# Kernel optimization log

Hardware: AMD Instinct MI355X
Metric: run time of the kernel (lower is better)

## Reference

```python
import jax, jax.numpy as jnp
import numpy as np

TOL = 1e-3

def _mask(x):
    # forward = relu, backward = identity (straight-through)
    return x + jax.lax.stop_gradient(jax.nn.relu(x) - x)

def setup_inputs() -> dict:
    key = jax.random.key(0)
    ks = jax.random.split(key, 6)
    B, L, A, Y = 4096, 64, 64, 128
    return {
        "LT": jax.random.uniform(ks[0], (B, L), jnp.float32),
        "K": jax.random.uniform(ks[1], (L, A), jnp.float32),
        "AT": jax.random.uniform(ks[2], (A,), jnp.float32),
        "u": jax.random.uniform(ks[3], (L * A, Y), jnp.float32),
        "e": jax.random.uniform(ks[4], (A, Y), jnp.float32),
        "b": jax.random.uniform(ks[5], (Y,), jnp.float32),
        "max_step": 50,
    }

def _fixed_point(LT3, AT3, Km, max_step):
    # LT3: [B,L,1], AT3: [A,1] (broadcasts over batch), Km: [L,A]
    B = LT3.shape[0]
    A = Km.shape[1]
    L = Km.shape[0]
    AF0 = jnp.zeros((B, A, 1), LT3.dtype)
    LF0 = jnp.zeros((B, L, 1), LT3.dtype)

    def step_fn(AF, LF):
        Ldi = LT3 / (jnp.matmul(Km, AF) + 1.0)          # [B,L,1]
        Adi = AT3 / (jnp.matmul(Km.T, LF) + 1.0)        # [B,A,1]
        AF_n = AT3 / (jnp.matmul(Km.T, Ldi) + 1.0)      # [B,A,1]
        LF_n = LT3 / (jnp.matmul(Km, Adi) + 1.0)        # [B,L,1]
        return AF_n, LF_n

    def cond(state):
        step, _, _, err = state
        return jnp.logical_and(step < max_step, err >= TOL)

    def body(state):
        step, AF, LF, _ = state
        AF_n, LF_n = step_fn(AF, LF)
        err = (jnp.max(jnp.abs(AF_n - AF) / (AF + 1e-5)) +
               jnp.max(jnp.abs(LF_n - LF) / (LF + 1e-5)))
        return (step + 1, AF_n, LF_n, err)

    _, AF, LF, _ = jax.lax.while_loop(cond, body, (0, AF0, LF0, jnp.array(jnp.inf, LT3.dtype)))
    return AF, LF

def reference(LT, K, AT, u, e, b, max_step):
    Km = _mask(K)            # [L,A]
    ATm = _mask(AT)          # [A]
    B = LT.shape[0]
    LT3 = LT[:, :, None]     # [B,L,1]
    AT3 = ATm[:, None]       # [A,1]

    # fixed-point loop was under torch.no_grad(): feed stop_gradient'd values
    AF, LF = _fixed_point(jax.lax.stop_gradient(LT3),
                          jax.lax.stop_gradient(AT3),
                          jax.lax.stop_gradient(Km), max_step)

    # final differentiable refinement step
    Ldi = LT3 / (jnp.matmul(Km, AF) + 1.0)
    Adi = AT3 / (jnp.matmul(Km.T, LF) + 1.0)
    AFf = AT3 / (jnp.matmul(Km.T, Ldi) + 1.0)   # [B,A,1]
    LFf = LT3 / (jnp.matmul(Km, Adi) + 1.0)     # [B,L,1]

    AFt = jnp.swapaxes(AFf, 1, 2)               # [B,1,A]
    D = (Km * jnp.matmul(LFf, AFt)).reshape(B, -1)   # [B, L*A]
    AFsq = AFt[:, 0, :]                          # [B,A]
    y = D @ u + AFsq @ e + b[None, :]            # [B,Y]
    return y
```

## Files before the change

### kernel.cpp

```cpp
#include <hip/hip_runtime.h>
#include <hip/hip_bf16.h>

typedef __bf16 bf16x8 __attribute__((ext_vector_type(8)));
typedef __bf16 bf16x4 __attribute__((ext_vector_type(4)));
typedef float  float4v __attribute__((ext_vector_type(4)));

#define MFMA16 __builtin_amdgcn_mfma_f32_16x16x32_bf16

__device__ __forceinline__ float bf2f(unsigned short u){
  union { unsigned int i; float f; } x; x.i = ((unsigned int)u) << 16; return x.f;
}
__device__ __forceinline__ unsigned short f2bf(float f){
  union { float f; unsigned int i; } x; x.f = f;
  unsigned int r = x.i + 0x7FFFu + ((x.i >> 16) & 1u);
  return (unsigned short)(r >> 16);
}
__device__ __forceinline__ float ldin(const void* p, int i, bool isbf){
  return isbf ? bf2f(((const unsigned short*)p)[i]) : ((const float*)p)[i];
}
__device__ __forceinline__ float frcp(float x){ return __builtin_amdgcn_rcpf(x); }

#define W2T_STRIDE 4160

__global__ __launch_bounds__(256) void k_prep(
    const void* K, const void* AT, const void* u, const void* e,
    const int* msin, __bf16* KmHi, __bf16* KTHi, __bf16* W2T, int* meta)
{
  int tid = threadIdx.x, bid = blockIdx.x;
  int ok = 0;
  if (tid < 64){
    float v = bf2f(((const unsigned short*)AT)[tid]);
    ok = (v >= 0.f && v <= 1.0f) ? 1 : 0;
  }
  int cnt = __syncthreads_count(ok);
  bool isbf = (cnt >= 60);

  if (bid < 256){
    int k0 = (bid >> 2) * 64, y0 = (bid & 3) * 32;
    __shared__ float sT[64 * 33];
    #pragma unroll
    for (int i = 0; i < 8; ++i){
      int flat = i * 256 + tid;
      int r = flat >> 5, c = flat & 31;
      sT[r * 33 + c] = ldin(u, (k0 + r) * 128 + (y0 + c), isbf);
    }
    __syncthreads();
    int l = k0 >> 6;
    #pragma unroll
    for (int i = 0; i < 8; ++i){
      int flat = i * 256 + tid;
      int yl = flat >> 6, kl = flat & 63;
      float km = ldin(K, l * 64 + kl, isbf); km = km > 0.f ? km : 0.f;
      W2T[(y0 + yl) * W2T_STRIDE + (k0 + kl)] = (__bf16)(km * sT[kl * 33 + yl]);
    }
  } else if (bid == 256){
    __shared__ float sK[64 * 65];
    #pragma unroll
    for (int i = 0; i < 16; ++i){
      int idx = i * 256 + tid;
      int l = idx >> 6, a = idx & 63;
      float v = ldin(K, idx, isbf); v = v > 0.f ? v : 0.f;
      sK[l * 65 + a] = v;
      KmHi[idx] = (__bf16)v;
    }
    __syncthreads();
    #pragma unroll
    for (int i = 0; i < 16; ++i){
      int idx = i * 256 + tid;
      int a = idx >> 6, l2 = idx & 63;
      KTHi[idx] = (__bf16)sK[l2 * 65 + a];
    }
    if (tid == 0){
      meta[0] = isbf ? 1 : 0;
      int mi = msin[0];
      if (mi <= 0 || mi > 1000000){
        float mf = ((const float*)msin)[0];
        mi = (mf > 0.f && mf < 1.0e6f) ? (int)mf : 50;
      }
      meta[1] = mi;
    }
  } else {
    __shared__ float sE[64 * 133];
    #pragma unroll
    for (int i = 0; i < 32; ++i){
      int idx = i * 256 + tid;
      int a = idx >> 7, y = idx & 127;
      sE[a * 133 + y] = ldin(e, idx, isbf);
    }
    __syncthreads();
    #pragma unroll
    for (int i = 0; i < 32; ++i){
      int idx = i * 256 + tid;
      int y = idx >> 6, a = idx & 63;
      W2T[y * W2T_STRIDE + 4096 + a] = (__bf16)sE[a * 133 + y];
    }
  }
}

template<bool SPLIT>
__device__ __forceinline__ void halfstep(
    const bf16x8 (&A)[4][2], const float4v (&V)[4],
    __bf16* sH, __bf16* sL, int rb, int wb)
{
  bf16x8 bh0 = *(const bf16x8*)(sH + rb);
  bf16x8 bh1 = *(const bf16x8*)(sH + rb + 32);
  const float4v ones = {1.f, 1.f, 1.f, 1.f};
  float4v c[4];
  #pragma unroll
  for (int T = 0; T < 4; ++T) c[T] = MFMA16(A[T][0], bh0, ones, 0, 0, 0);
  #pragma unroll
  for (int T = 0; T < 4; ++T) c[T] = MFMA16(A[T][1], bh1, c[T], 0, 0, 0);
  if (SPLIT){
    bf16x8 bl0 = *(const bf16x8*)(sL + rb);
    bf16x8 bl1 = *(const bf16x8*)(sL + rb + 32);
    const float4v zero = {0.f, 0.f, 0.f, 0.f};
    float4v d[4];
    #pragma unroll
    for (int T = 0; T < 4; ++T) d[T] = MFMA16(A[T][0], bl0, zero, 0, 0, 0);
    #pragma unroll
    for (int T = 0; T < 4; ++T) d[T] = MFMA16(A[T][1], bl1, d[T], 0, 0, 0);
    #pragma unroll
    for (int T = 0; T < 4; ++T) c[T] += d[T];
  }
  #pragma unroll
  for (int T = 0; T < 4; ++T){
    bf16x4 h, lo;
    #pragma unroll
    for (int r = 0; r < 4; ++r){
      float o = V[T][r] * frcp(c[T][r]);
      __bf16 hh = (__bf16)o;
      h[r] = hh;
      if (SPLIT) lo[r] = (__bf16)(o - (float)hh);
    }
    *(bf16x4*)(sH + wb + 16 * T) = h;
    if (SPLIT) *(bf16x4*)(sL + wb + 16 * T) = lo;
  }
}

__global__ __launch_bounds__(128, 1) void k_iter(
    const void* LT, const void* AT, const __bf16* KmHi, const __bf16* KTHi,
    const int* meta, __bf16* gAF, __bf16* gLF)
{
  __shared__ __attribute__((aligned(16))) __bf16 sHi[2][16 * 72];
  __shared__ __attribute__((aligned(16))) __bf16 sLo[2][16 * 72];
  const int tid = threadIdx.x, w = tid >> 6, lane = tid & 63;
  const int lr = lane & 15, q = lane >> 4;
  const int row0 = blockIdx.x * 16;
  __bf16* sH = sHi[w];
  __bf16* sL = sLo[w];

  const bf16x4 z4 = {(__bf16)0.f, (__bf16)0.f, (__bf16)0.f, (__bf16)0.f};
  for (int i = lane; i < 288; i += 64){
    *(bf16x4*)(sH + 4 * i) = z4;
    *(bf16x4*)(sL + 4 * i) = z4;
  }

  const int isbf = meta[0];
  const int ms   = meta[1];

  const __bf16* M1 = w ? KTHi : KmHi;
  const __bf16* M2 = w ? KmHi : KTHi;
  bf16x8 a1[4][2], a2[4][2];
  #pragma unroll
  for (int T = 0; T < 4; ++T)
    #pragma unroll
    for (int ks = 0; ks < 2; ++ks){
      int o = (16 * T + lr) * 64 + ks * 32 + q * 8;
      a1[T][ks] = *(const bf16x8*)(M1 + o);
      a2[T][ks] = *(const bf16x8*)(M2 + o);
    }

  float4v ltv[4], atv[4];
  if (isbf){
    const unsigned short* lt = (const unsigned short*)LT + (row0 + lr) * 64;
    const unsigned short* at = (const unsigned short*)AT;
    #pragma unroll
    for (int T = 0; T < 4; ++T)
      #pragma unroll
      for (int r = 0; r < 4; ++r){
        int d = 16 * T + q * 4 + r;
        ltv[T][r] = bf2f(lt[d]);
        atv[T][r] = fmaxf(bf2f(at[d]), 0.f);
      }
  } else {
    const float* lt = (const float*)LT + (row0 + lr) * 64;
    const float* at = (const float*)AT;
    #pragma unroll
    for (int T = 0; T < 4; ++T){
      ltv[T] = *(const float4v*)(lt + 16 * T + q * 4);
      float4v a = *(const float4v*)(at + 16 * T + q * 4);
      #pragma unroll
      for (int r = 0; r < 4; ++r) atv[T][r] = fmaxf(a[r], 0.f);
    }
  }
  float4v V1[4], V2[4];
  #pragma unroll
  for (int T = 0; T < 4; ++T){
    V1[T] = w ? atv[T] : ltv[T];
    V2[T] = w ? ltv[T] : atv[T];
  }

  const int rb = lr * 72 + q * 8;
  const int wb = lr * 72 + q * 4;

  const int nPlain = ms > 6 ? ms - 6 : 0;
  const int nSplit = ms - nPlain + 1;
  for (int s = 0; s < nPlain; ++s){
    halfstep<false>(a1, V1, sH, sL, rb, wb);
    halfstep<false>(a2, V2, sH, sL, rb, wb);
  }
  for (int s = 0; s < nSplit; ++s){
    halfstep<true>(a1, V1, sH, sL, rb, wb);
    halfstep<true>(a2, V2, sH, sL, rb, wb);
  }

  __bf16* gX = (w ? gLF : gAF) + row0 * 64;
  const int lrow = lane >> 2, seg = lane & 3;
  bf16x8 v0 = *(const bf16x8*)(sH + lrow * 72 + seg * 16);
  bf16x8 v1 = *(const bf16x8*)(sH + lrow * 72 + seg * 16 + 8);
  *(bf16x8*)(gX + lrow * 64 + seg * 16) = v0;
  *(bf16x8*)(gX + lrow * 64 + seg * 16 + 8) = v1;
}

__global__ __launch_bounds__(256) void k_epi(
    const __bf16* gAF, const __bf16* gLF, const __bf16* W2T,
    const void* bvec, const int* meta, void* out)
{
  __shared__ __attribute__((aligned(16))) __bf16 sAF[32 * 72], sLF[32 * 72];
  const int tid = threadIdx.x, wave = tid >> 6, lane = tid & 63;
  const int lr = lane & 15, q = lane >> 4;
  const int rg = blockIdx.x >> 1, yh = blockIdx.x & 1;
  const int row0 = rg * 32;
  const int isbf = meta[0];
  {
    int lrow = tid >> 3, seg = tid & 7;
    *(bf16x8*)(sAF + lrow * 72 + seg * 8) =
        *(const bf16x8*)(gAF + (row0 + lrow) * 64 + seg * 8);
    *(bf16x8*)(sLF + lrow * 72 + seg * 8) =
        *(const bf16x8*)(gLF + (row0 + lrow) * 64 + seg * 8);
  }
  __syncthreads();

  const int r0 = (wave & 1) * 16;
  const int y0 = yh * 64 + (wave >> 1) * 32;
  const int rloc = r0 + lr;

  const float bv0 = ldin(bvec, y0 + lr, isbf);
  const float bv1 = ldin(bvec, y0 + 16 + lr, isbf);
  float4v acc0 = {bv0, bv0, bv0, bv0};
  float4v acc1 = {bv1, bv1, bv1, bv1};

  bf16x8 af0 = *(const bf16x8*)(sAF + rloc * 72 + q * 8);
  bf16x8 af1 = *(const bf16x8*)(sAF + rloc * 72 + 32 + q * 8);
  float af0f[8], af1f[8];
  #pragma unroll
  for (int j = 0; j < 8; ++j){ af0f[j] = (float)af0[j]; af1f[j] = (float)af1[j]; }

  const __bf16* w0 = W2T + (y0 + lr) * W2T_STRIDE + q * 8;
  const __bf16* w1 = w0 + 16 * W2T_STRIDE;

  #pragma unroll 4
  for (int l = 0; l < 64; ++l){
    const float lf = (float)sLF[rloc * 72 + l];
    bf16x8 aD0, aD1;
    #pragma unroll
    for (int j = 0; j < 8; ++j){
      aD0[j] = (__bf16)(lf * af0f[j]);
      aD1[j] = (__bf16)(lf * af1f[j]);
    }
    const int kb = l * 64;
    bf16x8 b00 = *(const bf16x8*)(w0 + kb);
    bf16x8 b10 = *(const bf16x8*)(w1 + kb);
    bf16x8 b01 = *(const bf16x8*)(w0 + kb + 32);
    bf16x8 b11 = *(const bf16x8*)(w1 + kb + 32);
    acc0 = MFMA16(aD0, b00, acc0, 0, 0, 0);
    acc1 = MFMA16(aD0, b10, acc1, 0, 0, 0);
    acc0 = MFMA16(aD1, b01, acc0, 0, 0, 0);
    acc1 = MFMA16(aD1, b11, acc1, 0, 0, 0);
  }
  {
    bf16x8 b00 = *(const bf16x8*)(w0 + 4096);
    bf16x8 b10 = *(const bf16x8*)(w1 + 4096);
    bf16x8 b01 = *(const bf16x8*)(w0 + 4096 + 32);
    bf16x8 b11 = *(const bf16x8*)(w1 + 4096 + 32);
    acc0 = MFMA16(af0, b00, acc0, 0, 0, 0);
    acc1 = MFMA16(af0, b10, acc1, 0, 0, 0);
    acc0 = MFMA16(af1, b01, acc0, 0, 0, 0);
    acc1 = MFMA16(af1, b11, acc1, 0, 0, 0);
  }

  const int orow = row0 + r0 + q * 4;
  if (isbf){
    unsigned short* o = (unsigned short*)out;
    #pragma unroll
    for (int r = 0; r < 4; ++r){
      o[(orow + r) * 128 + y0 + lr]      = f2bf(acc0[r]);
      o[(orow + r) * 128 + y0 + 16 + lr] = f2bf(acc1[r]);
    }
  } else {
    float* o = (float*)out;
    #pragma unroll
    for (int r = 0; r < 4; ++r){
      o[(orow + r) * 128 + y0 + lr]      = acc0[r];
      o[(orow + r) * 128 + y0 + 16 + lr] = acc1[r];
    }
  }
}

extern "C" void kernel_launch(void* const* d_in, const int* in_sizes, int n_in,
                              void* d_out, int out_size, void* d_ws, size_t ws_size,
                              hipStream_t stream){
  char* ws = (char*)d_ws;
  int*    meta = (int*)ws;
  __bf16* KmHi = (__bf16*)(ws + 1024);
  __bf16* KTHi = (__bf16*)(ws + 9216);
  __bf16* gAF  = (__bf16*)(ws + 17408);
  __bf16* gLF  = (__bf16*)(ws + 541696);
  __bf16* W2T  = (__bf16*)(ws + 1065984);

  k_prep<<<dim3(258), dim3(256), 0, stream>>>(
      d_in[1], d_in[2], d_in[3], d_in[4], (const int*)d_in[6],
      KmHi, KTHi, W2T, meta);
  k_iter<<<dim3(256), dim3(128), 0, stream>>>(
      d_in[0], d_in[2], KmHi, KTHi, meta, gAF, gLF);
  k_epi<<<dim3(256), dim3(256), 0, stream>>>(
      gAF, gLF, W2T, d_in[5], meta, d_out);
}
```

Baseline: 142.4 us.

## Fuse prep into iteration kernel and double row tile in epilogue GEMM

The separate prep kernel is removed. Its work moves into extra blocks of the iteration kernel: W2T construction runs in blocks 256-385, and each iteration block builds its own Km/KmT fragments from shared memory, dropping one launch and the meta round-trip. The epilogue now processes 64 rows per block with two row tiles per wave, which reuses each W2T fragment load across twice as many MFMAs and halves the grid. Each epilogue block re-derives the dtype flag from the bias vector, and each iteration block redundantly reloads and transposes K.

```diff
diff --git a/kernel.cpp b/kernel.cpp
--- a/kernel.cpp
+++ b/kernel.cpp
@@ -6,6 +6,7 @@
 typedef float  float4v __attribute__((ext_vector_type(4)));
 
 #define MFMA16 __builtin_amdgcn_mfma_f32_16x16x32_bf16
+#define W2T_STRIDE 4160
 
 __device__ __forceinline__ float bf2f(unsigned short u){
   union { unsigned int i; float f; } x; x.i = ((unsigned int)u) << 16; return x.f;
@@ -20,82 +21,6 @@
 }
 __device__ __forceinline__ float frcp(float x){ return __builtin_amdgcn_rcpf(x); }
 
-#define W2T_STRIDE 4160
-
-__global__ __launch_bounds__(256) void k_prep(
-    const void* K, const void* AT, const void* u, const void* e,
-    const int* msin, __bf16* KmHi, __bf16* KTHi, __bf16* W2T, int* meta)
-{
-  int tid = threadIdx.x, bid = blockIdx.x;
-  int ok = 0;
-  if (tid < 64){
-    float v = bf2f(((const unsigned short*)AT)[tid]);
-    ok = (v >= 0.f && v <= 1.0f) ? 1 : 0;
-  }
-  int cnt = __syncthreads_count(ok);
-  bool isbf = (cnt >= 60);
-
-  if (bid < 256){
-    int k0 = (bid >> 2) * 64, y0 = (bid & 3) * 32;
-    __shared__ float sT[64 * 33];
-    #pragma unroll
-    for (int i = 0; i < 8; ++i){
-      int flat = i * 256 + tid;
-      int r = flat >> 5, c = flat & 31;
-      sT[r * 33 + c] = ldin(u, (k0 + r) * 128 + (y0 + c), isbf);
-    }
-    __syncthreads();
-    int l = k0 >> 6;
-    #pragma unroll
-    for (int i = 0; i < 8; ++i){
-      int flat = i * 256 + tid;
-      int yl = flat >> 6, kl = flat & 63;
-      float km = ldin(K, l * 64 + kl, isbf); km = km > 0.f ? km : 0.f;
-      W2T[(y0 + yl) * W2T_STRIDE + (k0 + kl)] = (__bf16)(km * sT[kl * 33 + yl]);
-    }
-  } else if (bid == 256){
-    __shared__ float sK[64 * 65];
-    #pragma unroll
-    for (int i = 0; i < 16; ++i){
-      int idx = i * 256 + tid;
-      int l = idx >> 6, a = idx & 63;
-      float v = ldin(K, idx, isbf); v = v > 0.f ? v : 0.f;
-      sK[l * 65 + a] = v;
-      KmHi[idx] = (__bf16)v;
-    }
-    __syncthreads();
-    #pragma unroll
-    for (int i = 0; i < 16; ++i){
-      int idx = i * 256 + tid;
-      int a = idx >> 6, l2 = idx & 63;
-      KTHi[idx] = (__bf16)sK[l2 * 65 + a];
-    }
-    if (tid == 0){
-      meta[0] = isbf ? 1 : 0;
-      int mi = msin[0];
-      if (mi <= 0 || mi > 1000000){
-        float mf = ((const float*)msin)[0];
-        mi = (mf > 0.f && mf < 1.0e6f) ? (int)mf : 50;
-      }
-      meta[1] = mi;
-    }
-  } else {
-    __shared__ float sE[64 * 133];
-    #pragma unroll
-    for (int i = 0; i < 32; ++i){
-      int idx = i * 256 + tid;
-      int a = idx >> 7, y = idx & 127;
-      sE[a * 133 + y] = ldin(e, idx, isbf);
-    }
-    __syncthreads();
-    #pragma unroll
-    for (int i = 0; i < 32; ++i){
-      int idx = i * 256 + tid;
-      int y = idx >> 6, a = idx & 63;
-      W2T[y * W2T_STRIDE + 4096 + a] = (__bf16)sE[a * 133 + y];
-    }
-  }
-}
 
 template<bool SPLIT>
 __device__ __forceinline__ void halfstep(
@@ -137,17 +62,77 @@
   }
 }
 
-__global__ __launch_bounds__(128, 1) void k_iter(
-    const void* LT, const void* AT, const __bf16* KmHi, const __bf16* KTHi,
-    const int* meta, __bf16* gAF, __bf16* gLF)
+__global__ __launch_bounds__(128) void k_fused(
+    const void* LT, const void* K, const void* AT, const void* u,
+    const void* e, const int* msin,
+    __bf16* gAF, __bf16* gLF, __bf16* W2T)
 {
-  __shared__ __attribute__((aligned(16))) __bf16 sHi[2][16 * 72];
-  __shared__ __attribute__((aligned(16))) __bf16 sLo[2][16 * 72];
-  const int tid = threadIdx.x, w = tid >> 6, lane = tid & 63;
+  __shared__ __attribute__((aligned(16))) char smem[25856];
+  const int tid = threadIdx.x, bid = blockIdx.x;
+
+  int ok = 0;
+  if (tid < 64){
+    float v = bf2f(((const unsigned short*)AT)[tid]);
+    ok = (v >= 0.f && v <= 1.0f) ? 1 : 0;
+  }
+  int cnt = __syncthreads_count(ok);
+  const bool isbf = (cnt >= 60);
+
+  if (bid >= 256){
+    if (bid < 384){
+      float* sT = (float*)smem;
+      const int ub = bid - 256;
+      const int kl = tid & 63;
+      for (int t2 = 0; t2 < 2; ++t2){
+        const int t = ub * 2 + t2;
+        const int k0 = (t >> 2) * 64, y0 = (t & 3) * 32, l = t >> 2;
+        __syncthreads();
+        #pragma unroll
+        for (int i = 0; i < 16; ++i){
+          int flat = i * 128 + tid, r = flat >> 5, c = flat & 31;
+          sT[r * 33 + c] = ldin(u, (k0 + r) * 128 + y0 + c, isbf);
+        }
+        __syncthreads();
+        float kmv = ldin(K, l * 64 + kl, isbf); kmv = fmaxf(kmv, 0.f);
+        #pragma unroll
+        for (int i = 0; i < 16; ++i){
+          int yl = 2 * i + (tid >> 6);
+          W2T[(y0 + yl) * W2T_STRIDE + k0 + kl] = (__bf16)(kmv * sT[kl * 33 + yl]);
+        }
+      }
+    } else {
+      float* sE = (float*)smem;
+      const int y0 = (bid - 384) * 64;
+      const int kl = tid & 63;
+      #pragma unroll
+      for (int i = 0; i < 32; ++i){
+        int flat = i * 128 + tid, a = flat >> 6, c = flat & 63;
+        sE[a * 65 + c] = ldin(e, a * 128 + y0 + c, isbf);
+      }
+      __syncthreads();
+      #pragma unroll
+      for (int i = 0; i < 32; ++i){
+        int yl = 2 * i + (tid >> 6);
+        W2T[(y0 + yl) * W2T_STRIDE + 4096 + kl] = (__bf16)sE[kl * 65 + yl];
+      }
+    }
+    return;
+  }
+
+  float* sKf = (float*)smem;
+  #pragma unroll
+  for (int i = 0; i < 32; ++i){
+    int idx = i * 128 + tid, l = idx >> 6, a = idx & 63;
+    float v = ldin(K, idx, isbf);
+    sKf[l * 65 + a] = fmaxf(v, 0.f);
+  }
+  __syncthreads();
+
+  const int w = tid >> 6, lane = tid & 63;
   const int lr = lane & 15, q = lane >> 4;
-  const int row0 = blockIdx.x * 16;
-  __bf16* sH = sHi[w];
-  __bf16* sL = sLo[w];
+  const int row0 = bid * 16;
+  __bf16* sH = (__bf16*)(smem + 16640 + w * 4608);
+  __bf16* sL = sH + 2304 / 2;
 
   const bf16x4 z4 = {(__bf16)0.f, (__bf16)0.f, (__bf16)0.f, (__bf16)0.f};
   for (int i = lane; i < 288; i += 64){
@@ -155,19 +140,20 @@
     *(bf16x4*)(sL + 4 * i) = z4;
   }
 
-  const int isbf = meta[0];
-  const int ms   = meta[1];
-
-  const __bf16* M1 = w ? KTHi : KmHi;
-  const __bf16* M2 = w ? KmHi : KTHi;
   bf16x8 a1[4][2], a2[4][2];
   #pragma unroll
   for (int T = 0; T < 4; ++T)
     #pragma unroll
     for (int ks = 0; ks < 2; ++ks){
-      int o = (16 * T + lr) * 64 + ks * 32 + q * 8;
-      a1[T][ks] = *(const bf16x8*)(M1 + o);
-      a2[T][ks] = *(const bf16x8*)(M2 + o);
+      bf16x8 f1, f2;
+      #pragma unroll
+      for (int j = 0; j < 8; ++j){
+        float vKm = sKf[(16 * T + lr) * 65 + ks * 32 + q * 8 + j];
+        float vKT = sKf[(ks * 32 + q * 8 + j) * 65 + 16 * T + lr];
+        f1[j] = (__bf16)(w ? vKT : vKm);
+        f2[j] = (__bf16)(w ? vKm : vKT);
+      }
+      a1[T][ks] = f1; a2[T][ks] = f2;
     }
 
   float4v ltv[4], atv[4];
@@ -200,11 +186,17 @@
     V2[T] = w ? ltv[T] : atv[T];
   }
 
+  int mi = msin[0];
+  if (mi <= 0 || mi > 1000000){
+    float mf = ((const float*)msin)[0];
+    mi = (mf > 0.f && mf < 1.0e6f) ? (int)mf : 50;
+  }
+
   const int rb = lr * 72 + q * 8;
   const int wb = lr * 72 + q * 4;
 
-  const int nPlain = ms > 6 ? ms - 6 : 0;
-  const int nSplit = ms - nPlain + 1;
+  const int nPlain = mi > 6 ? mi - 6 : 0;
+  const int nSplit = mi - nPlain;
   for (int s = 0; s < nPlain; ++s){
     halfstep<false>(a1, V1, sH, sL, rb, wb);
     halfstep<false>(a2, V2, sH, sL, rb, wb);
@@ -213,6 +205,8 @@
     halfstep<true>(a1, V1, sH, sL, rb, wb);
     halfstep<true>(a2, V2, sH, sL, rb, wb);
   }
+  halfstep<true>(a1, V1, sH, sL, rb, wb);
+  halfstep<true>(a2, V2, sH, sL, rb, wb);
 
   __bf16* gX = (w ? gLF : gAF) + row0 * 64;
   const int lrow = lane >> 2, seg = lane & 3;
@@ -224,86 +218,123 @@
 
 __global__ __launch_bounds__(256) void k_epi(
     const __bf16* gAF, const __bf16* gLF, const __bf16* W2T,
-    const void* bvec, const int* meta, void* out)
+    const void* bvec, void* out)
 {
-  __shared__ __attribute__((aligned(16))) __bf16 sAF[32 * 72], sLF[32 * 72];
-  const int tid = threadIdx.x, wave = tid >> 6, lane = tid & 63;
+  __shared__ __attribute__((aligned(16))) __bf16 sAF[64 * 72], sLF[64 * 72];
+  const int tid = threadIdx.x, wv = tid >> 6, lane = tid & 63;
   const int lr = lane & 15, q = lane >> 4;
+
+  int ok = 0;
+  if (tid < 64){
+    float v = bf2f(((const unsigned short*)bvec)[tid]);
+    ok = (v >= 0.f && v <= 1.0f) ? 1 : 0;
+  }
+  int cnt = __syncthreads_count(ok);
+  const bool isbf = (cnt >= 60);
+
   const int rg = blockIdx.x >> 1, yh = blockIdx.x & 1;
-  const int row0 = rg * 32;
-  const int isbf = meta[0];
+  const int rows0 = rg * 64;
   {
-    int lrow = tid >> 3, seg = tid & 7;
-    *(bf16x8*)(sAF + lrow * 72 + seg * 8) =
-        *(const bf16x8*)(gAF + (row0 + lrow) * 64 + seg * 8);
-    *(bf16x8*)(sLF + lrow * 72 + seg * 8) =
-        *(const bf16x8*)(gLF + (row0 + lrow) * 64 + seg * 8);
+    int lrow = tid >> 2, seg = tid & 3;
+    *(bf16x8*)(sAF + lrow * 72 + seg * 16) =
+        *(const bf16x8*)(gAF + (rows0 + lrow) * 64 + seg * 16);
+    *(bf16x8*)(sAF + lrow * 72 + seg * 16 + 8) =
+        *(const bf16x8*)(gAF + (rows0 + lrow) * 64 + seg * 16 + 8);
+    *(bf16x8*)(sLF + lrow * 72 + seg * 16) =
+        *(const bf16x8*)(gLF + (rows0 + lrow) * 64 + seg * 16);
+    *(bf16x8*)(sLF + lrow * 72 + seg * 16 + 8) =
+        *(const bf16x8*)(gLF + (rows0 + lrow) * 64 + seg * 16 + 8);
   }
   __syncthreads();
 
-  const int r0 = (wave & 1) * 16;
-  const int y0 = yh * 64 + (wave >> 1) * 32;
-  const int rloc = r0 + lr;
+  const int r0w = (wv & 1) * 32;
+  const int y0 = yh * 64 + (wv >> 1) * 32;
 
   const float bv0 = ldin(bvec, y0 + lr, isbf);
   const float bv1 = ldin(bvec, y0 + 16 + lr, isbf);
-  float4v acc0 = {bv0, bv0, bv0, bv0};
-  float4v acc1 = {bv1, bv1, bv1, bv1};
-
-  bf16x8 af0 = *(const bf16x8*)(sAF + rloc * 72 + q * 8);
-  bf16x8 af1 = *(const bf16x8*)(sAF + rloc * 72 + 32 + q * 8);
-  float af0f[8], af1f[8];
-  #pragma unroll
-  for (int j = 0; j < 8; ++j){ af0f[j] = (float)af0[j]; af1f[j] = (float)af1[j]; }
+  float4v acc[2][2];
+  acc[0][0] = float4v{bv0, bv0, bv0, bv0};
+  acc[0][1] = float4v{bv1, bv1, bv1, bv1};
+  acc[1][0] = acc[0][0];
+  acc[1][1] = acc[0][1];
+
+  bf16x8 afr[2][2];
+  float aff[2][2][8];
+  #pragma unroll
+  for (int at = 0; at < 2; ++at){
+    const int rloc = r0w + at * 16 + lr;
+    afr[at][0] = *(const bf16x8*)(sAF + rloc * 72 + q * 8);
+    afr[at][1] = *(const bf16x8*)(sAF + rloc * 72 + 32 + q * 8);
+    #pragma unroll
+    for (int j = 0; j < 8; ++j){
+      aff[at][0][j] = (float)afr[at][0][j];
+      aff[at][1][j] = (float)afr[at][1][j];
+    }
+  }
 
   const __bf16* w0 = W2T + (y0 + lr) * W2T_STRIDE + q * 8;
   const __bf16* w1 = w0 + 16 * W2T_STRIDE;
 
-  #pragma unroll 4
+  #pragma unroll 2
   for (int l = 0; l < 64; ++l){
-    const float lf = (float)sLF[rloc * 72 + l];
-    bf16x8 aD0, aD1;
+    const float lf0 = (float)sLF[(r0w + lr) * 72 + l];
+    const float lf1 = (float)sLF[(r0w + 16 + lr) * 72 + l];
+    bf16x8 aD[2][2];
     #pragma unroll
     for (int j = 0; j < 8; ++j){
-      aD0[j] = (__bf16)(lf * af0f[j]);
-      aD1[j] = (__bf16)(lf * af1f[j]);
+      aD[0][0][j] = (__bf16)(lf0 * aff[0][0][j]);
+      aD[0][1][j] = (__bf16)(lf0 * aff[0][1][j]);
+      aD[1][0][j] = (__bf16)(lf1 * aff[1][0][j]);
+      aD[1][1][j] = (__bf16)(lf1 * aff[1][1][j]);
     }
     const int kb = l * 64;
     bf16x8 b00 = *(const bf16x8*)(w0 + kb);
+    bf16x8 b01 = *(const bf16x8*)(w0 + kb + 32);
     bf16x8 b10 = *(const bf16x8*)(w1 + kb);
-    bf16x8 b01 = *(const bf16x8*)(w0 + kb + 32);
     bf16x8 b11 = *(const bf16x8*)(w1 + kb + 32);
-    acc0 = MFMA16(aD0, b00, acc0, 0, 0, 0);
-    acc1 = MFMA16(aD0, b10, acc1, 0, 0, 0);
-    acc0 = MFMA16(aD1, b01, acc0, 0, 0, 0);
-    acc1 = MFMA16(aD1, b11, acc1, 0, 0, 0);
+    acc[0][0] = MFMA16(aD[0][0], b00, acc[0][0], 0, 0, 0);
+    acc[0][0] = MFMA16(aD[0][1], b01, acc[0][0], 0, 0, 0);
+    acc[0][1] = MFMA16(aD[0][0], b10, acc[0][1], 0, 0, 0);
+    acc[0][1] = MFMA16(aD[0][1], b11, acc[0][1], 0, 0, 0);
+    acc[1][0] = MFMA16(aD[1][0], b00, acc[1][0], 0, 0, 0);
+    acc[1][0] = MFMA16(aD[1][1], b01, acc[1][0], 0, 0, 0);
+    acc[1][1] = MFMA16(aD[1][0], b10, acc[1][1], 0, 0, 0);
+    acc[1][1] = MFMA16(aD[1][1], b11, acc[1][1], 0, 0, 0);
   }
   {
     bf16x8 b00 = *(const bf16x8*)(w0 + 4096);
+    bf16x8 b01 = *(const bf16x8*)(w0 + 4096 + 32);
     bf16x8 b10 = *(const bf16x8*)(w1 + 4096);
-    bf16x8 b01 = *(const bf16x8*)(w0 + 4096 + 32);
     bf16x8 b11 = *(const bf16x8*)(w1 + 4096 + 32);
-    acc0 = MFMA16(af0, b00, acc0, 0, 0, 0);
-    acc1 = MFMA16(af0, b10, acc1, 0, 0, 0);
-    acc0 = MFMA16(af1, b01, acc0, 0, 0, 0);
-    acc1 = MFMA16(af1, b11, acc1, 0, 0, 0);
-  }
-
-  const int orow = row0 + r0 + q * 4;
+    #pragma unroll
+    for (int at = 0; at < 2; ++at){
+      acc[at][0] = MFMA16(afr[at][0], b00, acc[at][0], 0, 0, 0);
+      acc[at][0] = MFMA16(afr[at][1], b01, acc[at][0], 0, 0, 0);
+      acc[at][1] = MFMA16(afr[at][0], b10, acc[at][1], 0, 0, 0);
+      acc[at][1] = MFMA16(afr[at][1], b11, acc[at][1], 0, 0, 0);
+    }
+  }
+
   if (isbf){
     unsigned short* o = (unsigned short*)out;
     #pragma unroll
-    for (int r = 0; r < 4; ++r){
-      o[(orow + r) * 128 + y0 + lr]      = f2bf(acc0[r]);
-      o[(orow + r) * 128 + y0 + 16 + lr] = f2bf(acc1[r]);
-    }
+    for (int at = 0; at < 2; ++at)
+      #pragma unroll
+      for (int r = 0; r < 4; ++r){
+        int orow = rows0 + r0w + at * 16 + q * 4 + r;
+        o[orow * 128 + y0 + lr]      = f2bf(acc[at][0][r]);
+        o[orow * 128 + y0 + 16 + lr] = f2bf(acc[at][1][r]);
+      }
   } else {
     float* o = (float*)out;
     #pragma unroll
-    for (int r = 0; r < 4; ++r){
-      o[(orow + r) * 128 + y0 + lr]      = acc0[r];
-      o[(orow + r) * 128 + y0 + 16 + lr] = acc1[r];
-    }
+    for (int at = 0; at < 2; ++at)
+      #pragma unroll
+      for (int r = 0; r < 4; ++r){
+        int orow = rows0 + r0w + at * 16 + q * 4 + r;
+        o[orow * 128 + y0 + lr]      = acc[at][0][r];
+        o[orow * 128 + y0 + 16 + lr] = acc[at][1][r];
+      }
   }
 }
 
@@ -311,18 +342,13 @@
                               void* d_out, int out_size, void* d_ws, size_t ws_size,
                               hipStream_t stream){
   char* ws = (char*)d_ws;
-  int*    meta = (int*)ws;
-  __bf16* KmHi = (__bf16*)(ws + 1024);
-  __bf16* KTHi = (__bf16*)(ws + 9216);
-  __bf16* gAF  = (__bf16*)(ws + 17408);
-  __bf16* gLF  = (__bf16*)(ws + 541696);
-  __bf16* W2T  = (__bf16*)(ws + 1065984);
-
-  k_prep<<<dim3(258), dim3(256), 0, stream>>>(
-      d_in[1], d_in[2], d_in[3], d_in[4], (const int*)d_in[6],
-      KmHi, KTHi, W2T, meta);
-  k_iter<<<dim3(256), dim3(128), 0, stream>>>(
-      d_in[0], d_in[2], KmHi, KTHi, meta, gAF, gLF);
-  k_epi<<<dim3(256), dim3(256), 0, stream>>>(
-      gAF, gLF, W2T, d_in[5], meta, d_out);
-}
+  __bf16* gAF = (__bf16*)(ws);
+  __bf16* gLF = (__bf16*)(ws + 524288);
+  __bf16* W2T = (__bf16*)(ws + 1048576);
+
+  k_fused<<<dim3(386), dim3(128), 0, stream>>>(
+      d_in[0], d_in[1], d_in[2], d_in[3], d_in[4], (const int*)d_in[6],
+      gAF, gLF, W2T);
+  k_epi<<<dim3(128), dim3(256), 0, stream>>>(
+      gAF, gLF, W2T, d_in[5], d_out);
+}
```

After: 140.0 us. Within noise of the previous version (-1.7%).
